# Kernel tuning notes

Measured on AMD Instinct MI355X. Metric: run time of the kernel, lower is better.

The kernel has to match this reference:

```python
import jax, jax.numpy as jnp
import numpy as np

B, N, D, H = 2, 2048, 1024, 16
HD = D // H

def setup_inputs() -> dict:
    key = jax.random.key(0)
    ks = jax.random.split(key, 8)
    s = lambda fan_in: 1.0 / np.sqrt(fan_in)
    return {
        "x": jax.random.normal(ks[0], (B, N, D), jnp.float32),
        "coverage": jax.random.uniform(ks[1], (B, N, 1), jnp.float32),
        "w_qkv": jax.random.normal(ks[2], (D, 3 * D), jnp.float32) * s(D),
        "w_out": jax.random.normal(ks[3], (D, D), jnp.float32) * s(D),
        "b_out": jnp.zeros((D,), jnp.float32),
        "w_ce1": jax.random.normal(ks[4], (1, D // 4), jnp.float32),
        "b_ce1": jnp.zeros((D // 4,), jnp.float32),
        "w_ce2": jax.random.normal(ks[5], (D // 4, H), jnp.float32) * s(D // 4),
        "b_ce2": jnp.zeros((H,), jnp.float32),
        "w_fg1": jax.random.normal(ks[6], (D, D // 4), jnp.float32) * s(D),
        "b_fg1": jnp.zeros((D // 4,), jnp.float32),
        "w_fg2": jax.random.normal(ks[7], (D // 4, 1), jnp.float32) * s(D // 4),
        "b_fg2": jnp.zeros((1,), jnp.float32),
    }

def reference(x, coverage, w_qkv, w_out, b_out, w_ce1, b_ce1, w_ce2, b_ce2,
              w_fg1, b_fg1, w_fg2, b_fg2):
    b, n, d = x.shape
    h = w_ce2.shape[1]
    hd = d // h
    scale = hd ** -0.5
    qkv = x @ w_qkv  # (B,N,3D)
    q, k, v = jnp.split(qkv, 3, axis=-1)
    q = q.reshape(b, n, h, hd).transpose(0, 2, 1, 3)  # (B,H,N,hd)
    k = k.reshape(b, n, h, hd).transpose(0, 2, 1, 3)
    v = v.reshape(b, n, h, hd).transpose(0, 2, 1, 3)
    attn = jnp.einsum("bhnd,bhmd->bhnm", q, k) * scale  # (B,H,N,N)
    # coverage bias: MLP(1 -> D/4 -> H), broadcast over query dim
    cov = jax.nn.silu(coverage @ w_ce1 + b_ce1) @ w_ce2 + b_ce2  # (B,N,H)
    cov_bias = cov.transpose(0, 2, 1)[:, :, None, :]  # (B,H,1,N)
    # fusion gate on mean-pooled features
    x_pooled = x.mean(axis=1)  # (B,D)
    g = jax.nn.sigmoid(jax.nn.silu(x_pooled @ w_fg1 + b_fg1) @ w_fg2 + b_fg2)  # (B,1)
    g = g[:, :, None, None]  # (B,1,1,1)
    # g*(attn+bias) + (1-g)*attn == attn + g*bias (exact same math)
    attn = attn + g * cov_bias
    attn = jax.nn.softmax(attn, axis=-1)
    out = jnp.einsum("bhnm,bhmd->bhnd", attn, v)  # (B,H,N,hd)
    out = out.transpose(0, 2, 1, 3).reshape(b, n, d)
    return out @ w_out + b_out
```

## Files before the change

### kernel.cpp

```cpp
#include <hip/hip_runtime.h>
#include <math.h>

typedef __bf16 bf16_t;
typedef __bf16 bf16x8 __attribute__((ext_vector_type(8)));
typedef __bf16 bf16x4 __attribute__((ext_vector_type(4)));
typedef float f32x4 __attribute__((ext_vector_type(4)));

#define MFMA16(a, b, c) __builtin_amdgcn_mfma_f32_16x16x32_bf16((a), (b), (c), 0, 0, 0)

constexpr int Bc = 2, Nc = 2048, Dc = 1024, Hc = 16, HDc = 64;
constexpr float C1 = 0.18033688011112042f;
constexpr float LOG2E = 1.4426950408889634f;

__device__ __forceinline__ void glds16(const bf16_t* g, bf16_t* l) {
    __builtin_amdgcn_global_load_lds(
        (const __attribute__((address_space(1))) unsigned int*)g,
        (__attribute__((address_space(3))) unsigned int*)l, 16, 0, 0);
}

__device__ __forceinline__ void tr64_body(const float* __restrict__ src,
                                          bf16_t* __restrict__ dst, int R, int C,
                                          int bx, int by, bf16_t* tile, int t) {
    int r0 = by * 64, c0 = bx * 64;
    int cl = t & 63, rl = t >> 6;
#pragma unroll
    for (int p = 0; p < 16; ++p) {
        int r = p * 4 + rl;
        tile[r * 66 + cl] = (bf16_t)src[(size_t)(r0 + r) * C + c0 + cl];
    }
    __syncthreads();
#pragma unroll
    for (int p = 0; p < 16; ++p) {
        int r = p * 4 + rl;
        dst[(size_t)(c0 + r) * R + r0 + cl] = tile[cl * 66 + r];
    }
}

__global__ __launch_bounds__(256) void prep(const float* __restrict__ x,
                                            bf16_t* __restrict__ Xb,
                                            const float* __restrict__ w_qkv,
                                            bf16_t* __restrict__ Wt,
                                            const float* __restrict__ w_out,
                                            bf16_t* __restrict__ WoT,
                                            float* __restrict__ pooled,
                                            const float* __restrict__ coverage,
                                            const float* __restrict__ w_ce1,
                                            const float* __restrict__ b_ce1,
                                            const float* __restrict__ w_ce2,
                                            const float* __restrict__ b_ce2,
                                            float* __restrict__ cbias) {
    __shared__ __align__(16) float smem[8768];
    int bid = blockIdx.x, t = threadIdx.x;

    if (bid < 64) {
        float* w1s = smem;
        float* b1s = smem + 256;
        float* w2s = smem + 512;
        float* part = smem + 4608;
        int b = bid >> 5, n0 = (bid & 31) * 64;
        w1s[t] = w_ce1[t];
        b1s[t] = b_ce1[t];
        {
            float4* w2v = (float4*)w2s;
            const float4* g4 = (const float4*)w_ce2;
#pragma unroll
            for (int i = 0; i < 4; ++i) w2v[i * 256 + t] = g4[i * 256 + t];
        }
        __syncthreads();
        int wv = t >> 6, lane2 = t & 63;
        float c = coverage[b * 2048 + n0 + lane2];
        float acc[16];
#pragma unroll
        for (int hh = 0; hh < 16; ++hh) acc[hh] = 0.f;
        for (int jj = 0; jj < 64; ++jj) {
            int j = wv * 64 + jj;
            float tv = fmaf(c, w1s[j], b1s[j]);
            tv = tv / (1.0f + __expf(-tv));
#pragma unroll
            for (int hh = 0; hh < 16; ++hh)
                acc[hh] = fmaf(tv, w2s[j * 16 + hh], acc[hh]);
        }
#pragma unroll
        for (int hh = 0; hh < 16; ++hh) part[lane2 * 65 + wv * 16 + hh] = acc[hh];
        __syncthreads();
#pragma unroll
        for (int i = 0; i < 4; ++i) {
            int idx = t + i * 256;
            int nl = idx >> 4, hh = idx & 15;
            const float* pr = part + nl * 65 + hh;
            float s = pr[0] + pr[16] + pr[32] + pr[48];
            cbias[((size_t)b * 16 + hh) * 2048 + n0 + nl] = LOG2E * (s + b_ce2[hh]);
        }
    } else if (bid < 832) {
        int bb = bid - 64;
        tr64_body(w_qkv, Wt, 1024, 3072, bb % 48, bb / 48, (bf16_t*)smem, t);
    } else if (bid < 1088) {
        int bb = bid - 832;
        tr64_body(w_out, WoT, 1024, 1024, bb & 15, bb >> 4, (bf16_t*)smem, t);
    } else {
        int blk = bid - 1088;
        int b = blk >> 7;
        int rbase = blk * 16;
        int d = t * 4;
        float s0 = 0.f, s1 = 0.f, s2 = 0.f, s3 = 0.f;
        for (int rr = 0; rr < 16; ++rr) {
            size_t off = (size_t)(rbase + rr) * 1024 + d;
            float4 v = *(const float4*)(x + off);
            s0 += v.x; s1 += v.y; s2 += v.z; s3 += v.w;
            bf16x4 o = { (bf16_t)v.x, (bf16_t)v.y, (bf16_t)v.z, (bf16_t)v.w };
            *(bf16x4*)(Xb + off) = o;
        }
        atomicAdd(&pooled[b * 1024 + d + 0], s0);
        atomicAdd(&pooled[b * 1024 + d + 1], s1);
        atomicAdd(&pooled[b * 1024 + d + 2], s2);
        atomicAdd(&pooled[b * 1024 + d + 3], s3);
    }
}

__global__ __launch_bounds__(512, 2) void qkv_gemm(const bf16_t* __restrict__ Xb,
                                                   const bf16_t* __restrict__ Wt,
                                                   bf16_t* __restrict__ Q,
                                                   bf16_t* __restrict__ Kb,
                                                   bf16_t* __restrict__ Vt,
                                                   const float* __restrict__ pooled,
                                                   const float* __restrict__ w_fg1,
                                                   const float* __restrict__ b_fg1,
                                                   const float* __restrict__ w_fg2,
                                                   float* __restrict__ hacc) {
    __shared__ __align__(16) bf16_t lds[2][16384];
    int t = threadIdx.x;

    if (blockIdx.y == 12) {
        float* red = (float*)&lds[0][0];
        int blk = blockIdx.x;
        int b = blk >> 3, jb = (blk & 7) * 32;
        for (int jj = 0; jj < 32; ++jj) {
            int j = jb + jj;
            int d = t * 2;
            float p = pooled[b * 1024 + d] * w_fg1[d * 256 + j]
                    + pooled[b * 1024 + d + 1] * w_fg1[(d + 1) * 256 + j];
#pragma unroll
            for (int off = 32; off > 0; off >>= 1) p += __shfl_down(p, off);
            if ((t & 63) == 0) red[t >> 6] = p;
            __syncthreads();
            if (t == 0) {
                float s = red[0] + red[1] + red[2] + red[3]
                        + red[4] + red[5] + red[6] + red[7];
                float hj = s * (1.0f / 2048.0f) + b_fg1[j];
                hj = hj / (1.0f + __expf(-hj));
                atomicAdd(&hacc[b], hj * w_fg2[j]);
            }
            __syncthreads();
        }
        return;
    }

    int w = t >> 6, lane = t & 63;
    int l16 = lane & 15, quad = lane >> 4;
    int wm = w >> 2, wn = w & 3;
    int m0 = blockIdx.x * 256;
    int n0 = blockIdx.y * 256;
    f32x4 acc[8][4] = {};
    int sw = (l16 >> 2) & 3;
    int cq = (quad ^ sw) * 8;

    int srow[4], ssc[4], sdst[4];
    bool sB[4];
#pragma unroll
    for (int j = 0; j < 4; ++j) {
        int off = w * 4096 + j * 1024 + lane * 16;
        bool inB = off >= 16384;
        int o2 = off - (inB ? 16384 : 0);
        int row = o2 >> 6;
        int ch = (o2 >> 4) & 3;
        srow[j] = row;
        ssc[j] = ch ^ ((row >> 2) & 3);
        sB[j] = inB;
        sdst[j] = (w * 4096 + j * 1024) >> 1;
    }
    auto stg = [&](int j, int k0, int bf) {
        const bf16_t* src = sB[j] ? Xb + (size_t)(m0 + srow[j]) * 1024
                                  : Wt + (size_t)(n0 + srow[j]) * 1024;
        glds16(src + k0 + ssc[j] * 8, &lds[bf][sdst[j]]);
    };

    int aB = (wm * 128 + l16) * 32 + cq;
    int bB = 8192 + (wn * 64 + l16) * 32 + cq;

    stg(0, 0, 0); stg(1, 0, 0); stg(2, 0, 0); stg(3, 0, 0);

#pragma unroll 1
    for (int ks = 0; ks < 32; ++ks) {
        int cb = ks & 1, k0n = (ks + 1) * 32;
        if (ks + 1 < 32) {
            stg(0, k0n, cb ^ 1); stg(1, k0n, cb ^ 1);
            asm volatile("s_waitcnt vmcnt(2)" ::: "memory");
        } else {
            asm volatile("s_waitcnt vmcnt(0)" ::: "memory");
        }
        __builtin_amdgcn_s_barrier();
        __builtin_amdgcn_sched_barrier(0);

        const bf16_t* L = lds[cb];
        bf16x8 Ar[4], Br[4];
#pragma unroll
        for (int mi = 0; mi < 4; ++mi) Ar[mi] = *(const bf16x8*)(L + aB + mi * 512);
#pragma unroll
        for (int ni = 0; ni < 4; ++ni) Br[ni] = *(const bf16x8*)(L + bB + ni * 512);
        __builtin_amdgcn_s_setprio(1);
#pragma unroll
        for (int mi = 0; mi < 4; ++mi)
#pragma unroll
            for (int ni = 0; ni < 4; ++ni)
                acc[mi][ni] = MFMA16(Ar[mi], Br[ni], acc[mi][ni]);
        __builtin_amdgcn_s_setprio(0);
        __builtin_amdgcn_s_barrier();
        __builtin_amdgcn_sched_barrier(0);

        if (ks + 1 < 32) { stg(2, k0n, cb ^ 1); stg(3, k0n, cb ^ 1); }
#pragma unroll
        for (int mi = 0; mi < 4; ++mi) Ar[mi] = *(const bf16x8*)(L + aB + 2048 + mi * 512);
        __builtin_amdgcn_s_setprio(1);
#pragma unroll
        for (int mi = 0; mi < 4; ++mi)
#pragma unroll
            for (int ni = 0; ni < 4; ++ni)
                acc[4 + mi][ni] = MFMA16(Ar[mi], Br[ni], acc[4 + mi][ni]);
        __builtin_amdgcn_s_setprio(0);
        __builtin_amdgcn_s_barrier();
        __builtin_amdgcn_sched_barrier(0);
    }

    int sec = n0 >> 10;
    float scq = (sec == 0) ? C1 : 1.0f;
#pragma unroll
    for (int mi = 0; mi < 8; ++mi) {
        int gc = n0 + wm * 128 + mi * 16 + quad * 4;
        int dcol = gc & 1023;
        int h = dcol >> 6, hd = dcol & 63;
#pragma unroll
        for (int ni = 0; ni < 4; ++ni) {
            int gx = m0 + wn * 64 + ni * 16 + l16;
            int b = gx >> 11, n = gx & 2047;
            size_t bh = (size_t)(b * 16 + h);
            if (sec == 2) {
#pragma unroll
                for (int r = 0; r < 4; ++r)
                    Vt[(bh * 64 + hd + r) * 2048 + n] = (bf16_t)acc[mi][ni][r];
            } else {
                bf16x4 pk = { (bf16_t)(acc[mi][ni][0] * scq), (bf16_t)(acc[mi][ni][1] * scq),
                              (bf16_t)(acc[mi][ni][2] * scq), (bf16_t)(acc[mi][ni][3] * scq) };
                bf16_t* dst = (sec == 0 ? Q : Kb);
                *(bf16x4*)(dst + (bh * 2048 + n) * 64 + hd) = pk;
            }
        }
    }
}

__global__ __launch_bounds__(256) void attn_k(const bf16_t* __restrict__ Q,
                                              const bf16_t* __restrict__ Kb,
                                              const bf16_t* __restrict__ Vt,
                                              const float* __restrict__ cbias,
                                              const float* __restrict__ hacc,
                                              const float* __restrict__ b_fg2,
                                              bf16_t* __restrict__ O) {
    __shared__ __align__(16) bf16_t kbuf[2][2][64 * 64];
    __shared__ __align__(16) bf16_t vbuf[2][2][64 * 64];
    __shared__ __align__(16) float ball[2048];
    int t = threadIdx.x, w = t >> 6, lane = t & 63;
    int l16 = lane & 15, quad = lane >> 4;
    int id = blockIdx.x;
    int xcd = id & 7, slot = id >> 3;
    int bh = xcd * 4 + (slot >> 4);
    int xblk = slot & 15;
    int b = bh >> 4, h = bh & 15;
    int qa = xblk * 128 + w * 32;
    const bf16_t* Qh = Q + (size_t)bh * 2048 * 64;
    const bf16_t* Kh = Kb + (size_t)bh * 2048 * 64;
    const bf16_t* Vh = Vt + (size_t)bh * 64 * 2048;
    const float* bih = cbias + (size_t)bh * 2048;
    float g = 1.0f / (1.0f + __expf(-(hacc[b] + b_fg2[0])));

#pragma unroll
    for (int c = 0; c < 2; ++c) {
        float4 v = *(const float4*)(bih + c * 1024 + t * 4);
        float4 sv = { v.x * g, v.y * g, v.z * g, v.w * g };
        *(float4*)(ball + c * 1024 + t * 4) = sv;
    }

    int fb0 = w * 2048, fb1 = fb0 + 1024;
    int f0 = fb0 + lane * 16, f1 = fb1 + lane * 16;
    int krow0 = f0 >> 7, kch0 = ((f0 >> 4) & 7) ^ (krow0 & 7);
    int krow1 = f1 >> 7, kch1 = ((f1 >> 4) & 7) ^ (krow1 & 7);

    bf16x8 qf[2][2];
#pragma unroll
    for (int qt = 0; qt < 2; ++qt)
#pragma unroll
        for (int dh = 0; dh < 2; ++dh)
            qf[qt][dh] = *(const bf16x8*)(Qh + (size_t)(qa + qt * 16 + l16) * 64 + dh * 32 + quad * 8);

    f32x4 o[2][4] = {};
    f32x4 lacc[2] = {};
    bf16x8 onesb;
#pragma unroll
    for (int i = 0; i < 8; ++i) onesb[i] = (bf16_t)1.0f;
    int swl = l16 & 7;
    int qh = quad >> 1, ql = quad & 1;

    int bk0 = l16 * 64 + ((quad ^ swl) * 8);
    int bk1 = l16 * 64 + (((4 + quad) ^ swl) * 8);
    int bv0 = l16 * 64 + ql * 4 + ((qh ^ swl) * 8);
    int bv1 = l16 * 64 + ql * 4 + (((2 + qh) ^ swl) * 8);
    int bv2 = l16 * 64 + ql * 4 + (((4 + qh) ^ swl) * 8);
    int bv3 = l16 * 64 + ql * 4 + (((6 + qh) ^ swl) * 8);

    auto stageSub = [&](int jn, bf16_t* kd, bf16_t* vd) {
        glds16(Kh + (size_t)(jn + krow0) * 64 + kch0 * 8, kd + (fb0 >> 1));
        glds16(Kh + (size_t)(jn + krow1) * 64 + kch1 * 8, kd + (fb1 >> 1));
        glds16(Vh + (size_t)krow0 * 2048 + jn + kch0 * 8, vd + (fb0 >> 1));
        glds16(Vh + (size_t)krow1 * 2048 + jn + kch1 * 8, vd + (fb1 >> 1));
    };
    auto stage = [&](int tile_, int bf) {
        int jn = tile_ * 128;
        stageSub(jn,      &kbuf[bf][0][0], &vbuf[bf][0][0]);
        stageSub(jn + 64, &kbuf[bf][1][0], &vbuf[bf][1][0]);
    };

    auto exppack = [&](f32x4 (&s)[2][4], bf16x8 (&pf)[2][2]) {
#pragma unroll
        for (int qt = 0; qt < 2; ++qt) {
#pragma unroll
            for (int kt = 0; kt < 4; ++kt)
#pragma unroll
                for (int r = 0; r < 4; ++r)
                    s[qt][kt][r] = __builtin_amdgcn_exp2f(s[qt][kt][r]);
#pragma unroll
            for (int pv = 0; pv < 2; ++pv) {
                bf16x8 tmp;
#pragma unroll
                for (int i = 0; i < 4; ++i) {
                    tmp[i]     = (bf16_t)s[qt][2 * pv][i];
                    tmp[i + 4] = (bf16_t)s[qt][2 * pv + 1][i];
                }
                pf[qt][pv] = tmp;
            }
        }
    };
    auto pvacc = [&](const bf16_t* vb, bf16x8 (&pf)[2][2]) {
#pragma unroll
        for (int qt = 0; qt < 2; ++qt) {
            lacc[qt] = MFMA16(pf[qt][0], onesb, lacc[qt]);
            lacc[qt] = MFMA16(pf[qt][1], onesb, lacc[qt]);
        }
#pragma unroll
        for (int dt = 0; dt < 4; ++dt) {
            bf16x4 va0 = *(const bf16x4*)(vb + dt * 1024 + bv0);
            bf16x4 vc0 = *(const bf16x4*)(vb + dt * 1024 + bv1);
            bf16x8 vf0 = __builtin_shufflevector(va0, vc0, 0, 1, 2, 3, 4, 5, 6, 7);
            bf16x4 va1 = *(const bf16x4*)(vb + dt * 1024 + bv2);
            bf16x4 vc1 = *(const bf16x4*)(vb + dt * 1024 + bv3);
            bf16x8 vf1 = __builtin_shufflevector(va1, vc1, 0, 1, 2, 3, 4, 5, 6, 7);
#pragma unroll
            for (int qt = 0; qt < 2; ++qt) {
                o[qt][dt] = MFMA16(pf[qt][0], vf0, o[qt][dt]);
                o[qt][dt] = MFMA16(pf[qt][1], vf1, o[qt][dt]);
            }
        }
    };

    stage(0, 0);

    for (int it = 0; it < 16; ++it) {
        int sel = it & 1;
        asm volatile("s_waitcnt lgkmcnt(0)" ::: "memory");
        __builtin_amdgcn_s_barrier();
        if (it + 1 < 16) {
            stage(it + 1, sel ^ 1);
            asm volatile("s_waitcnt vmcnt(8)" ::: "memory");
        } else {
            asm volatile("s_waitcnt vmcnt(0)" ::: "memory");
        }
        __builtin_amdgcn_s_barrier();
        __builtin_amdgcn_sched_barrier(0);

        f32x4 s[2][2][4];
        __builtin_amdgcn_s_setprio(1);
#pragma unroll
        for (int sub = 0; sub < 2; ++sub) {
            int j0 = it * 128 + sub * 64;
            const bf16_t* kb = &kbuf[sel][sub][0];
#pragma unroll
            for (int kt = 0; kt < 4; ++kt) {
                f32x4 bi = *(const f32x4*)(ball + j0 + kt * 16 + quad * 4);
                bf16x8 kf0 = *(const bf16x8*)(kb + kt * 1024 + bk0);
                bf16x8 kf1 = *(const bf16x8*)(kb + kt * 1024 + bk1);
#pragma unroll
                for (int qt = 0; qt < 2; ++qt) {
                    s[sub][qt][kt] = MFMA16(kf0, qf[qt][0], bi);
                    s[sub][qt][kt] = MFMA16(kf1, qf[qt][1], s[sub][qt][kt]);
                }
            }
        }
        __builtin_amdgcn_s_setprio(0);

        bf16x8 pf0[2][2], pf1[2][2];
        exppack(s[0], pf0);
        __builtin_amdgcn_s_setprio(1);
        pvacc(&vbuf[sel][0][0], pf0);
        __builtin_amdgcn_s_setprio(0);
        exppack(s[1], pf1);
        __builtin_amdgcn_s_setprio(1);
        pvacc(&vbuf[sel][1][0], pf1);
        __builtin_amdgcn_s_setprio(0);
    }

#pragma unroll
    for (int qt = 0; qt < 2; ++qt) {
        f32x4 rinv;
#pragma unroll
        for (int r = 0; r < 4; ++r) rinv[r] = 1.0f / lacc[qt][r];
#pragma unroll
        for (int dt = 0; dt < 4; ++dt)
#pragma unroll
            for (int r = 0; r < 4; ++r) {
                int row = qa + qt * 16 + quad * 4 + r;
                O[(size_t)(b * 2048 + row) * 1024 + h * 64 + dt * 16 + l16] =
                    (bf16_t)(o[qt][dt][r] * rinv[r]);
            }
    }
}

__global__ __launch_bounds__(256) void out_gemm(const bf16_t* __restrict__ A,
                                                const bf16_t* __restrict__ Wt,
                                                const float* __restrict__ bias,
                                                float* __restrict__ Cout) {
    __shared__ __align__(16) bf16_t At[2][64 * 32];
    __shared__ __align__(16) bf16_t Bt[2][128 * 32];
    int t = threadIdx.x, w = t >> 6, lane = t & 63;
    int l16 = lane & 15, quad = lane >> 4;
    int wm = w & 1, wx = w >> 1;
    int m0 = blockIdx.x * 128;
    int n0 = blockIdx.y * 64;
    f32x4 acc[2][4] = {};
    int sw = (l16 >> 2) & 3;
    int cq = (quad ^ sw) * 8;

    int ao = w * 1024 + lane * 16;
    int arow = ao >> 6, ach = (ao >> 4) & 3;
    int asc = ach ^ ((arow >> 2) & 3);
    int adst = (w * 1024) >> 1;
    int brow[2], bsc[2], bdst[2];
#pragma unroll
    for (int i = 0; i < 2; ++i) {
        int bo = w * 2048 + i * 1024 + lane * 16;
        int row = bo >> 6, ch = (bo >> 4) & 3;
        brow[i] = row;
        bsc[i] = ch ^ ((row >> 2) & 3);
        bdst[i] = (w * 2048 + i * 1024) >> 1;
    }
    auto stage = [&](int k0, int bf) {
        glds16(Wt + (size_t)(n0 + arow) * 1024 + k0 + asc * 8, At[bf] + adst);
#pragma unroll
        for (int i = 0; i < 2; ++i)
            glds16(A + (size_t)(m0 + brow[i]) * 1024 + k0 + bsc[i] * 8, Bt[bf] + bdst[i]);
    };

    stage(0, 0);
    for (int ks = 0; ks < 32; ++ks) {
        int sel = ks & 1;
        asm volatile("s_waitcnt lgkmcnt(0)" ::: "memory");
        __builtin_amdgcn_s_barrier();
        if (ks + 1 < 32) {
            stage((ks + 1) * 32, sel ^ 1);
            asm volatile("s_waitcnt vmcnt(3)" ::: "memory");
        } else {
            asm volatile("s_waitcnt vmcnt(0)" ::: "memory");
        }
        __builtin_amdgcn_s_barrier();
        __builtin_amdgcn_sched_barrier(0);

        const bf16_t* Ab = At[sel];
        const bf16_t* Bb = Bt[sel];
        bf16x8 afr[2], bfr[4];
#pragma unroll
        for (int mi = 0; mi < 2; ++mi)
            afr[mi] = *(const bf16x8*)(Ab + (wx * 32 + mi * 16 + l16) * 32 + cq);
#pragma unroll
        for (int ni = 0; ni < 4; ++ni)
            bfr[ni] = *(const bf16x8*)(Bb + (wm * 64 + ni * 16 + l16) * 32 + cq);
        __builtin_amdgcn_s_setprio(1);
#pragma unroll
        for (int mi = 0; mi < 2; ++mi)
#pragma unroll
            for (int ni = 0; ni < 4; ++ni)
                acc[mi][ni] = MFMA16(afr[mi], bfr[ni], acc[mi][ni]);
        __builtin_amdgcn_s_setprio(0);
    }

#pragma unroll
    for (int mi = 0; mi < 2; ++mi) {
        int gc = n0 + wx * 32 + mi * 16 + quad * 4;
        float4 bv = *(const float4*)(bias + gc);
#pragma unroll
        for (int ni = 0; ni < 4; ++ni) {
            int gx = m0 + wm * 64 + ni * 16 + l16;
            float4 ov = { acc[mi][ni][0] + bv.x, acc[mi][ni][1] + bv.y,
                          acc[mi][ni][2] + bv.z, acc[mi][ni][3] + bv.w };
            *(float4*)(Cout + (size_t)gx * 1024 + gc) = ov;
        }
    }
}

extern "C" void kernel_launch(void* const* d_in, const int* in_sizes, int n_in,
                              void* d_out, int out_size, void* d_ws, size_t ws_size,
                              hipStream_t stream) {
    const float* x     = (const float*)d_in[0];
    const float* cov   = (const float*)d_in[1];
    const float* w_qkv = (const float*)d_in[2];
    const float* w_out = (const float*)d_in[3];
    const float* b_out = (const float*)d_in[4];
    const float* w_ce1 = (const float*)d_in[5];
    const float* b_ce1 = (const float*)d_in[6];
    const float* w_ce2 = (const float*)d_in[7];
    const float* b_ce2 = (const float*)d_in[8];
    const float* w_fg1 = (const float*)d_in[9];
    const float* b_fg1 = (const float*)d_in[10];
    const float* w_fg2 = (const float*)d_in[11];
    const float* b_fg2 = (const float*)d_in[12];

    char* ws = (char*)d_ws;
    bf16_t* Wt     = (bf16_t*)(ws);
    bf16_t* WoT    = (bf16_t*)(ws + 6291456);
    bf16_t* Xb     = (bf16_t*)(ws + 8388608);
    bf16_t* Qb     = (bf16_t*)(ws + 16777216);
    bf16_t* Kbb    = (bf16_t*)(ws + 25165824);
    bf16_t* Vt     = (bf16_t*)(ws + 33554432);
    bf16_t* Ob     = (bf16_t*)(ws + 41943040);
    float*  pooled = (float*)(ws + 50331648);
    float*  hacc   = (float*)(ws + 50339840);
    float*  biasb  = (float*)(ws + 50340096);

    hipMemsetAsync(pooled, 0, 8200, stream);
    prep<<<1344, 256, 0, stream>>>(x, Xb, w_qkv, Wt, w_out, WoT, pooled,
                                   cov, w_ce1, b_ce1, w_ce2, b_ce2, biasb);
    qkv_gemm<<<dim3(16, 13), 512, 0, stream>>>(Xb, Wt, Qb, Kbb, Vt,
                                               pooled, w_fg1, b_fg1, w_fg2, hacc);
    attn_k<<<512, 256, 0, stream>>>(Qb, Kbb, Vt, biasb, hacc, b_fg2, Ob);
    out_gemm<<<dim3(32, 16), 256, 0, stream>>>(Ob, WoT, b_out, (float*)d_out);
}
```

Baseline: 227.6 us.

## Halve attention query tile per block and double grid to 1024 blocks

Each wave of the attention kernel now handles 16 query rows instead of 32, and each iteration processes one 64-key tile instead of two. The grid doubles to 1024 blocks and LDS use per block halves. The aim is more parallelism and occupancy with fewer registers per wave. The cost is that every K/V tile loaded into LDS is reused by half as many queries, so global and LDS traffic per FLOP doubles, and there are twice as many barriers per unit of work.

```diff
diff --git a/kernel.cpp b/kernel.cpp
--- a/kernel.cpp
+++ b/kernel.cpp
@@ -264,17 +264,17 @@
                                               const float* __restrict__ hacc,
                                               const float* __restrict__ b_fg2,
                                               bf16_t* __restrict__ O) {
-    __shared__ __align__(16) bf16_t kbuf[2][2][64 * 64];
-    __shared__ __align__(16) bf16_t vbuf[2][2][64 * 64];
+    __shared__ __align__(16) bf16_t kbuf[2][64 * 64];
+    __shared__ __align__(16) bf16_t vbuf[2][64 * 64];
     __shared__ __align__(16) float ball[2048];
     int t = threadIdx.x, w = t >> 6, lane = t & 63;
     int l16 = lane & 15, quad = lane >> 4;
     int id = blockIdx.x;
     int xcd = id & 7, slot = id >> 3;
-    int bh = xcd * 4 + (slot >> 4);
-    int xblk = slot & 15;
+    int bh = xcd * 4 + (slot >> 5);
+    int xblk = slot & 31;
     int b = bh >> 4, h = bh & 15;
-    int qa = xblk * 128 + w * 32;
+    int qa = xblk * 64 + w * 16;
     const bf16_t* Qh = Q + (size_t)bh * 2048 * 64;
     const bf16_t* Kh = Kb + (size_t)bh * 2048 * 64;
     const bf16_t* Vh = Vt + (size_t)bh * 64 * 2048;
@@ -293,15 +293,13 @@
     int krow0 = f0 >> 7, kch0 = ((f0 >> 4) & 7) ^ (krow0 & 7);
     int krow1 = f1 >> 7, kch1 = ((f1 >> 4) & 7) ^ (krow1 & 7);
 
-    bf16x8 qf[2][2];
-#pragma unroll
-    for (int qt = 0; qt < 2; ++qt)
-#pragma unroll
-        for (int dh = 0; dh < 2; ++dh)
-            qf[qt][dh] = *(const bf16x8*)(Qh + (size_t)(qa + qt * 16 + l16) * 64 + dh * 32 + quad * 8);
-
-    f32x4 o[2][4] = {};
-    f32x4 lacc[2] = {};
+    bf16x8 qf[2];
+#pragma unroll
+    for (int dh = 0; dh < 2; ++dh)
+        qf[dh] = *(const bf16x8*)(Qh + (size_t)(qa + l16) * 64 + dh * 32 + quad * 8);
+
+    f32x4 o[4] = {};
+    f32x4 lacc = {};
     bf16x8 onesb;
 #pragma unroll
     for (int i = 0; i < 8; ++i) onesb[i] = (bf16_t)1.0f;
@@ -315,44 +313,64 @@
     int bv2 = l16 * 64 + ql * 4 + (((4 + qh) ^ swl) * 8);
     int bv3 = l16 * 64 + ql * 4 + (((6 + qh) ^ swl) * 8);
 
-    auto stageSub = [&](int jn, bf16_t* kd, bf16_t* vd) {
-        glds16(Kh + (size_t)(jn + krow0) * 64 + kch0 * 8, kd + (fb0 >> 1));
-        glds16(Kh + (size_t)(jn + krow1) * 64 + kch1 * 8, kd + (fb1 >> 1));
-        glds16(Vh + (size_t)krow0 * 2048 + jn + kch0 * 8, vd + (fb0 >> 1));
-        glds16(Vh + (size_t)krow1 * 2048 + jn + kch1 * 8, vd + (fb1 >> 1));
+    auto stage = [&](int tile_, int bf) {
+        int jn = tile_ * 64;
+        glds16(Kh + (size_t)(jn + krow0) * 64 + kch0 * 8, &kbuf[bf][fb0 >> 1]);
+        glds16(Kh + (size_t)(jn + krow1) * 64 + kch1 * 8, &kbuf[bf][fb1 >> 1]);
+        glds16(Vh + (size_t)krow0 * 2048 + jn + kch0 * 8, &vbuf[bf][fb0 >> 1]);
+        glds16(Vh + (size_t)krow1 * 2048 + jn + kch1 * 8, &vbuf[bf][fb1 >> 1]);
     };
-    auto stage = [&](int tile_, int bf) {
-        int jn = tile_ * 128;
-        stageSub(jn,      &kbuf[bf][0][0], &vbuf[bf][0][0]);
-        stageSub(jn + 64, &kbuf[bf][1][0], &vbuf[bf][1][0]);
-    };
-
-    auto exppack = [&](f32x4 (&s)[2][4], bf16x8 (&pf)[2][2]) {
-#pragma unroll
-        for (int qt = 0; qt < 2; ++qt) {
-#pragma unroll
-            for (int kt = 0; kt < 4; ++kt)
-#pragma unroll
-                for (int r = 0; r < 4; ++r)
-                    s[qt][kt][r] = __builtin_amdgcn_exp2f(s[qt][kt][r]);
-#pragma unroll
-            for (int pv = 0; pv < 2; ++pv) {
-                bf16x8 tmp;
-#pragma unroll
-                for (int i = 0; i < 4; ++i) {
-                    tmp[i]     = (bf16_t)s[qt][2 * pv][i];
-                    tmp[i + 4] = (bf16_t)s[qt][2 * pv + 1][i];
-                }
-                pf[qt][pv] = tmp;
+
+    stage(0, 0);
+
+    for (int it = 0; it < 32; ++it) {
+        int sel = it & 1, j0 = it * 64;
+        asm volatile("s_waitcnt lgkmcnt(0)" ::: "memory");
+        __builtin_amdgcn_s_barrier();
+        if (it + 1 < 32) {
+            stage(it + 1, sel ^ 1);
+            asm volatile("s_waitcnt vmcnt(4)" ::: "memory");
+        } else {
+            asm volatile("s_waitcnt vmcnt(0)" ::: "memory");
+        }
+        __builtin_amdgcn_s_barrier();
+        __builtin_amdgcn_sched_barrier(0);
+
+        const bf16_t* kb = &kbuf[sel][0];
+        const bf16_t* vb = &vbuf[sel][0];
+
+        f32x4 s[4];
+        __builtin_amdgcn_s_setprio(1);
+#pragma unroll
+        for (int kt = 0; kt < 4; ++kt) {
+            f32x4 bi = *(const f32x4*)(ball + j0 + kt * 16 + quad * 4);
+            bf16x8 kf0 = *(const bf16x8*)(kb + kt * 1024 + bk0);
+            bf16x8 kf1 = *(const bf16x8*)(kb + kt * 1024 + bk1);
+            s[kt] = MFMA16(kf0, qf[0], bi);
+            s[kt] = MFMA16(kf1, qf[1], s[kt]);
+        }
+        __builtin_amdgcn_s_setprio(0);
+
+        bf16x8 pf[2];
+#pragma unroll
+        for (int kt = 0; kt < 4; ++kt)
+#pragma unroll
+            for (int r = 0; r < 4; ++r)
+                s[kt][r] = __builtin_amdgcn_exp2f(s[kt][r]);
+#pragma unroll
+        for (int pv = 0; pv < 2; ++pv) {
+            bf16x8 tmp;
+#pragma unroll
+            for (int i = 0; i < 4; ++i) {
+                tmp[i]     = (bf16_t)s[2 * pv][i];
+                tmp[i + 4] = (bf16_t)s[2 * pv + 1][i];
             }
-        }
-    };
-    auto pvacc = [&](const bf16_t* vb, bf16x8 (&pf)[2][2]) {
-#pragma unroll
-        for (int qt = 0; qt < 2; ++qt) {
-            lacc[qt] = MFMA16(pf[qt][0], onesb, lacc[qt]);
-            lacc[qt] = MFMA16(pf[qt][1], onesb, lacc[qt]);
-        }
+            pf[pv] = tmp;
+        }
+
+        __builtin_amdgcn_s_setprio(1);
+        lacc = MFMA16(pf[0], onesb, lacc);
+        lacc = MFMA16(pf[1], onesb, lacc);
 #pragma unroll
         for (int dt = 0; dt < 4; ++dt) {
             bf16x4 va0 = *(const bf16x4*)(vb + dt * 1024 + bv0);
@@ -361,74 +379,23 @@
             bf16x4 va1 = *(const bf16x4*)(vb + dt * 1024 + bv2);
             bf16x4 vc1 = *(const bf16x4*)(vb + dt * 1024 + bv3);
             bf16x8 vf1 = __builtin_shufflevector(va1, vc1, 0, 1, 2, 3, 4, 5, 6, 7);
-#pragma unroll
-            for (int qt = 0; qt < 2; ++qt) {
-                o[qt][dt] = MFMA16(pf[qt][0], vf0, o[qt][dt]);
-                o[qt][dt] = MFMA16(pf[qt][1], vf1, o[qt][dt]);
-            }
-        }
-    };
-
-    stage(0, 0);
-
-    for (int it = 0; it < 16; ++it) {
-        int sel = it & 1;
-        asm volatile("s_waitcnt lgkmcnt(0)" ::: "memory");
-        __builtin_amdgcn_s_barrier();
-        if (it + 1 < 16) {
-            stage(it + 1, sel ^ 1);
-            asm volatile("s_waitcnt vmcnt(8)" ::: "memory");
-        } else {
-            asm volatile("s_waitcnt vmcnt(0)" ::: "memory");
-        }
-        __builtin_amdgcn_s_barrier();
-        __builtin_amdgcn_sched_barrier(0);
-
-        f32x4 s[2][2][4];
-        __builtin_amdgcn_s_setprio(1);
-#pragma unroll
-        for (int sub = 0; sub < 2; ++sub) {
-            int j0 = it * 128 + sub * 64;
-            const bf16_t* kb = &kbuf[sel][sub][0];
-#pragma unroll
-            for (int kt = 0; kt < 4; ++kt) {
-                f32x4 bi = *(const f32x4*)(ball + j0 + kt * 16 + quad * 4);
-                bf16x8 kf0 = *(const bf16x8*)(kb + kt * 1024 + bk0);
-                bf16x8 kf1 = *(const bf16x8*)(kb + kt * 1024 + bk1);
-#pragma unroll
-                for (int qt = 0; qt < 2; ++qt) {
-                    s[sub][qt][kt] = MFMA16(kf0, qf[qt][0], bi);
-                    s[sub][qt][kt] = MFMA16(kf1, qf[qt][1], s[sub][qt][kt]);
-                }
-            }
+            o[dt] = MFMA16(pf[0], vf0, o[dt]);
+            o[dt] = MFMA16(pf[1], vf1, o[dt]);
         }
         __builtin_amdgcn_s_setprio(0);
-
-        bf16x8 pf0[2][2], pf1[2][2];
-        exppack(s[0], pf0);
-        __builtin_amdgcn_s_setprio(1);
-        pvacc(&vbuf[sel][0][0], pf0);
-        __builtin_amdgcn_s_setprio(0);
-        exppack(s[1], pf1);
-        __builtin_amdgcn_s_setprio(1);
-        pvacc(&vbuf[sel][1][0], pf1);
-        __builtin_amdgcn_s_setprio(0);
-    }
-
-#pragma unroll
-    for (int qt = 0; qt < 2; ++qt) {
-        f32x4 rinv;
-#pragma unroll
-        for (int r = 0; r < 4; ++r) rinv[r] = 1.0f / lacc[qt][r];
-#pragma unroll
-        for (int dt = 0; dt < 4; ++dt)
-#pragma unroll
-            for (int r = 0; r < 4; ++r) {
-                int row = qa + qt * 16 + quad * 4 + r;
-                O[(size_t)(b * 2048 + row) * 1024 + h * 64 + dt * 16 + l16] =
-                    (bf16_t)(o[qt][dt][r] * rinv[r]);
-            }
-    }
+    }
+
+    f32x4 rinv;
+#pragma unroll
+    for (int r = 0; r < 4; ++r) rinv[r] = 1.0f / lacc[r];
+#pragma unroll
+    for (int dt = 0; dt < 4; ++dt)
+#pragma unroll
+        for (int r = 0; r < 4; ++r) {
+            int row = qa + quad * 4 + r;
+            O[(size_t)(b * 2048 + row) * 1024 + h * 64 + dt * 16 + l16] =
+                (bf16_t)(o[dt][r] * rinv[r]);
+        }
 }
 
 __global__ __launch_bounds__(256) void out_gemm(const bf16_t* __restrict__ A,
@@ -546,6 +513,6 @@
                                    cov, w_ce1, b_ce1, w_ce2, b_ce2, biasb);
     qkv_gemm<<<dim3(16, 13), 512, 0, stream>>>(Xb, Wt, Qb, Kbb, Vt,
                                                pooled, w_fg1, b_fg1, w_fg2, hacc);
-    attn_k<<<512, 256, 0, stream>>>(Qb, Kbb, Vt, biasb, hacc, b_fg2, Ob);
+    attn_k<<<1024, 256, 0, stream>>>(Qb, Kbb, Vt, biasb, hacc, b_fg2, Ob);
     out_gemm<<<dim3(32, 16), 256, 0, stream>>>(Ob, WoT, b_out, (float*)d_out);
 }
```

New measurement: 234.6 us. 3.1% more time.
